# Performance work log

Measured on AMD Instinct MI355X. Metric: run time of the kernel, lower is better.

Reference implementation:

```python
import jax, jax.numpy as jnp
import numpy as np

EPS_NORM = 1e-12
RMS_EPS = 1e-5


def _rmsnorm(x, w):
    var = jnp.mean(jnp.square(x), axis=-1, keepdims=True)
    return x * jax.lax.rsqrt(var + RMS_EPS) * w


def setup_inputs() -> dict:
    key = jax.random.key(0)
    B, T, D, H, R, K = 2, 512, 1024, 16, 32, 3
    d = D // H
    ks = jax.random.split(key, 11)
    s = 0.02
    return dict(
        x=jax.random.normal(ks[0], (B, T, D), jnp.float32),
        Wq=jax.random.normal(ks[1], (D, D), jnp.float32) * s,
        Wk=jax.random.normal(ks[2], (D, D), jnp.float32) * s,
        Wv=jax.random.normal(ks[3], (D, D), jnp.float32) * s,
        Wo=jax.random.normal(ks[4], (D, D), jnp.float32) * s,
        wA=jax.random.normal(ks[5], (D, R), jnp.float32) * s,
        wB=jax.random.normal(ks[6], (R, D), jnp.float32) * s,
        conv_w=jax.random.normal(ks[7], (D, K), jnp.float32) * 0.5,
        beta_w=jax.random.normal(ks[8], (D, H), jnp.float32) * s,
        g_w=jax.random.normal(ks[9], (D, H), jnp.float32) * s,
        g_b=jnp.zeros((H,), jnp.float32),
        qnorm_w=jnp.ones((d,), jnp.float32),
        knorm_w=jnp.ones((d,), jnp.float32),
    )


def _path_attention(x, Wq, Wk, Wv, Wo, wA, wB, conv_w, beta_w, g_w, g_b, qnorm_w, knorm_w):
    # PaTH attention: s_ij = q_i^T (H_i ... H_{j+1}) k_j / sqrt(d) + (G_i - G_j),
    # H_t = I - beta_t w_t w_t^T (unit w_t), G = cumsum(logsigmoid(forget gate)).
    B, T, D = x.shape
    d = qnorm_w.shape[0]
    H = D // d
    scale = d ** -0.5

    q = (x @ Wq).reshape(B, T, H, d)
    k = (x @ Wk).reshape(B, T, H, d)
    v = (x @ Wv).reshape(B, T, H, d)

    # low-rank W projection + causal depthwise short conv (size 3) + silu
    w = (x @ wA) @ wB                                      # [B,T,D]
    wp = jnp.pad(w, ((0, 0), (2, 0), (0, 0)))
    w = wp[:, 0:T] * conv_w[:, 0] + wp[:, 1:T + 1] * conv_w[:, 1] + wp[:, 2:T + 2] * conv_w[:, 2]
    w = jax.nn.silu(w).reshape(B, T, H, d)
    # unit Householder directions
    w = w * jax.lax.rsqrt(jnp.sum(jnp.square(w), -1, keepdims=True) + EPS_NORM)

    beta = 2.0 * jax.nn.sigmoid(x @ beta_w)                # [B,T,H], in (0,2)
    g = jax.nn.log_sigmoid(x @ g_w + g_b)                  # [B,T,H] forget gate, log-space

    q = _rmsnorm(q, qnorm_w)
    k = _rmsnorm(k, knorm_w)

    # -> [B,H,T,(d)]
    q, k, v, w = (t.transpose(0, 2, 1, 3) for t in (q, k, v, w))
    beta = beta.transpose(0, 2, 1)
    g = g.transpose(0, 2, 1)

    # UT/WY form: A_{t,j} = w_t . (H_{t-1}...H_{j+1} k_j), t > j, via unit-lower tri solve:
    #   A_{t,j} + sum_{s<t} beta_s (w_t.w_s) A_{s,j} = (w_t.k_j) [t>j]
    tri_s = jnp.tril(jnp.ones((T, T), bool), -1)
    C = jnp.einsum('bhtd,bhsd->bhts', w, w) * beta[:, :, None, :]
    L = jnp.where(tri_s, C, 0.0) + jnp.eye(T, dtype=x.dtype)
    Rhs = jnp.where(tri_s, jnp.einsum('bhtd,bhjd->bhtj', w, k), 0.0)
    A = jax.scipy.linalg.solve_triangular(L, Rhs, lower=True, unit_diagonal=True)

    # s_ij = q_i.k_j - sum_{j<t<=i} (q_i.w_t) beta_t A_{t,j}
    tri = jnp.tril(jnp.ones((T, T), bool))
    qw = jnp.where(tri, jnp.einsum('bhid,bhtd->bhit', q, w), 0.0)
    S = jnp.einsum('bhid,bhjd->bhij', q, k) - jnp.einsum('bhit,bhtj->bhij', qw, beta[..., None] * A)

    G = jnp.cumsum(g, axis=-1)                             # [B,H,T]
    logits = S * scale + (G[..., :, None] - G[..., None, :])
    logits = jnp.where(tri, logits, -1e30)
    P = jax.nn.softmax(logits, axis=-1)
    o = jnp.einsum('bhij,bhjd->bhid', P, v)
    return o.transpose(0, 2, 1, 3).reshape(B, T, D) @ Wo


def reference(x, Wq, Wk, Wv, Wo, wA, wB, conv_w, beta_w, g_w, g_b, qnorm_w, knorm_w):
    return _path_attention(x, Wq, Wk, Wv, Wo, wA, wB, conv_w, beta_w, g_w, g_b, qnorm_w, knorm_w)
```

## Files before the change

### kernel.cpp

```cpp
#include <hip/hip_runtime.h>
#include <hip/hip_bf16.h>
#include <math.h>

#define B_ 2
#define T_ 512
#define D_ 1024
#define H_ 16
#define R_ 32
#define DH 64
#define BT_ (B_*T_)
#define BH_ (B_*H_)

typedef __attribute__((ext_vector_type(8))) short bf16x8;
typedef __attribute__((ext_vector_type(4))) short s16x4;
typedef __attribute__((ext_vector_type(4))) float f32x4;

#define MFMA_BF16(a, b, c) __builtin_amdgcn_mfma_f32_16x16x32_bf16(a, b, c, 0, 0, 0)

static __device__ __forceinline__ short bf16s(float v) {
  __hip_bfloat16 b = __float2bfloat16(v);
  return *reinterpret_cast<short*>(&b);
}
static __device__ __forceinline__ float b2f(__hip_bfloat16 h) { return __bfloat162float(h); }

__device__ __forceinline__ bf16x8 ldfrag(const __hip_bfloat16 s[][72], int b16, int kb, int fr, int kq) {
  return *(const bf16x8*)&s[b16 * 16 + fr][kb * 32 + kq * 8];
}
__device__ __forceinline__ void stage64(const __hip_bfloat16* __restrict__ g, int ldg,
                                        __hip_bfloat16 s[][72], int tid) {
#pragma unroll
  for (int l = 0; l < 2; ++l) {
    int f = tid + l * 256;
    int r = f >> 3, c = (f & 7) << 3;
    *(int4*)&s[r][c] = *(const int4*)&g[(size_t)r * ldg + c];
  }
}

typedef const __attribute__((address_space(1))) void* as1cv;
typedef __attribute__((address_space(3))) void* as3v;
__device__ __forceinline__ void gl16(const __hip_bfloat16* g, __hip_bfloat16* l) {
  __builtin_amdgcn_global_load_lds((as1cv)g, (as3v)l, 16, 0, 0);
}
__device__ __forceinline__ void stage64s(const __hip_bfloat16* __restrict__ g, int ldg,
                                         __hip_bfloat16* s, int tid) {
#pragma unroll
  for (int i = 0; i < 2; ++i) {
    int chunk = tid + i * 256;
    int r = chunk >> 3, c8 = (chunk & 7) ^ (r & 7);
    gl16(g + (size_t)r * ldg + c8 * 8, s + chunk * 8);
  }
}
__device__ __forceinline__ bf16x8 ldfragS(const __hip_bfloat16* s, int b16, int half, int fr, int kq) {
  int r = b16 * 16 + fr;
  int col8 = ((kq + half * 4) ^ (r & 7)) * 8;
  return *(const bf16x8*)&s[r * 64 + col8];
}

__global__ __launch_bounds__(256) void prep_k(const float* __restrict__ x,
                                              const float* __restrict__ Wq,
                                              const float* __restrict__ Wk,
                                              const float* __restrict__ Wv,
                                              const float* __restrict__ Wo,
                                              const float* __restrict__ wA,
                                              const float* __restrict__ bw,
                                              const float* __restrict__ gw,
                                              __hip_bfloat16* __restrict__ xhi,
                                              __hip_bfloat16* __restrict__ xlo,
                                              __hip_bfloat16* __restrict__ wqkvT,
                                              __hip_bfloat16* __restrict__ woT,
                                              __hip_bfloat16* __restrict__ wcThi,
                                              __hip_bfloat16* __restrict__ wcTlo) {
  __shared__ float tile[64][65];
  const int bid = blockIdx.x, tid = threadIdx.x;
  if (bid < 512) {
    int i8 = bid * 256 + tid;
    float4 v0 = ((const float4*)x)[i8 * 2];
    float4 v1 = ((const float4*)x)[i8 * 2 + 1];
    float c[8] = {v0.x, v0.y, v0.z, v0.w, v1.x, v1.y, v1.z, v1.w};
    bf16x8 ph, pl;
#pragma unroll
    for (int u = 0; u < 8; ++u) {
      __hip_bfloat16 h = __float2bfloat16(c[u]);
      ph[u] = *reinterpret_cast<short*>(&h);
      pl[u] = bf16s(c[u] - __bfloat162float(h));
    }
    *(bf16x8*)&xhi[(size_t)i8 * 8] = ph;
    *(bf16x8*)&xlo[(size_t)i8 * 8] = pl;
  } else if (bid < 1536) {
    const int zz = (bid - 512) >> 8, idx = (bid - 512) & 255;
    const float* Wm = (zz == 0) ? Wq : (zz == 1) ? Wk : (zz == 2) ? Wv : Wo;
    __hip_bfloat16* thi = (zz < 3) ? (wqkvT + (size_t)zz * 1024 * D_) : woT;
    const int bn = (idx & 15) * 64, bk = (idx >> 4) * 64;
#pragma unroll
    for (int l = 0; l < 4; ++l) {
      int f = tid + l * 256; int r = f >> 4, c = (f & 15) << 2;
      *(float4*)&tile[r][c] = *(const float4*)&Wm[(size_t)(bk + r) * D_ + bn + c];
    }
    __syncthreads();
#pragma unroll
    for (int l = 0; l < 4; ++l) {
      int f = tid + l * 256; int n = f >> 4, k0 = (f & 15) << 2;
      s16x4 ph;
#pragma unroll
      for (int u = 0; u < 4; ++u) ph[u] = bf16s(tile[k0 + u][n]);
      *(s16x4*)&thi[(size_t)(bn + n) * D_ + bk + k0] = ph;
    }
  } else {
    int n = bid - 1536;
    for (int k = tid; k < D_; k += 256) {
      float v;
      if (n < 32) v = wA[(size_t)k * R_ + n];
      else if (n < 48) v = bw[(size_t)k * H_ + (n - 32)];
      else v = gw[(size_t)k * H_ + (n - 48)];
      __hip_bfloat16 h = __float2bfloat16(v);
      wcThi[(size_t)n * D_ + k] = h;
      wcTlo[(size_t)n * D_ + k] = __float2bfloat16(v - __bfloat162float(h));
    }
  }
}

__global__ __launch_bounds__(256) void gemm_qkv(const __hip_bfloat16* __restrict__ ah,
                                                const __hip_bfloat16* __restrict__ bT,
                                                __hip_bfloat16* __restrict__ qb,
                                                __hip_bfloat16* __restrict__ kb,
                                                __hip_bfloat16* __restrict__ vhi,
                                                const float* __restrict__ qnw,
                                                const float* __restrict__ knw) {
  __shared__ __hip_bfloat16 As[2][64][64];
  __shared__ __hip_bfloat16 Bs[2][64][64];
  __shared__ __hip_bfloat16 Lt[64][72];
  const int bm = blockIdx.y * 64, bn = blockIdx.x * 64;
  const int tid = threadIdx.x, w = tid >> 6, lane = tid & 63;
  const int fr = lane & 15, kq = lane >> 4;
  const f32x4 zf = {0.f, 0.f, 0.f, 0.f};
  f32x4 acc[4] = {zf, zf, zf, zf};
  const __hip_bfloat16* ap = ah + (size_t)bm * D_;
  const __hip_bfloat16* bp = bT + (size_t)bn * D_;
  stage64s(ap, D_, &As[0][0][0], tid);
  stage64s(bp, D_, &Bs[0][0][0], tid);
  __syncthreads();
  for (int t = 0; t < 16; ++t) {
    const int cur = t & 1;
    if (t < 15) {
      stage64s(ap + (t + 1) * 64, D_, &As[cur ^ 1][0][0], tid);
      stage64s(bp + (t + 1) * 64, D_, &Bs[cur ^ 1][0][0], tid);
    }
    bf16x8 a0 = ldfragS(&As[cur][0][0], w, 0, fr, kq);
    bf16x8 a1 = ldfragS(&As[cur][0][0], w, 1, fr, kq);
#pragma unroll
    for (int n = 0; n < 4; ++n) {
      acc[n] = MFMA_BF16(a0, ldfragS(&Bs[cur][0][0], n, 0, fr, kq), acc[n]);
      acc[n] = MFMA_BF16(a1, ldfragS(&Bs[cur][0][0], n, 1, fr, kq), acc[n]);
    }
    __syncthreads();
  }

  if (bn < 2048) {
    float rs[4];
#pragma unroll
    for (int reg = 0; reg < 4; ++reg) {
      float s = 0.f;
#pragma unroll
      for (int n = 0; n < 4; ++n) s += acc[n][reg] * acc[n][reg];
#pragma unroll
      for (int mm = 1; mm <= 8; mm <<= 1) s += __shfl_xor(s, mm);
      rs[reg] = rsqrtf(s * (1.f / DH) + 1e-5f);
    }
    const bool isq = (bn < 1024);
    __hip_bfloat16* outp = isq ? qb : kb;
#pragma unroll
    for (int n = 0; n < 4; ++n) {
      int gn = bn + n * 16 + fr;
      int dd = gn & 63, h = (gn & 1023) >> 6;
      float nw = (isq ? qnw : knw)[dd];
#pragma unroll
      for (int reg = 0; reg < 4; ++reg) {
        int gm = bm + w * 16 + kq * 4 + reg;
        int bb = gm >> 9, tt = gm & 511;
        outp[(((size_t)(bb * H_ + h)) * T_ + tt) * DH + dd] =
            __float2bfloat16(acc[n][reg] * rs[reg] * nw);
      }
    }
  } else {
    const int row0 = w * 16 + kq * 4;
#pragma unroll
    for (int n = 0; n < 4; ++n) {
      int dd = n * 16 + fr;
#pragma unroll
      for (int reg = 0; reg < 4; ++reg) Lt[dd][row0 + reg] = __float2bfloat16(acc[n][reg]);
    }
    __syncthreads();
    const int b = bm >> 9, t0 = bm & 511, h = (bn - 2048) >> 6;
    const size_t base = ((size_t)(b * H_ + h)) * DH * T_;
#pragma unroll
    for (int l = 0; l < 2; ++l) {
      int f = tid + l * 256;
      int dd = f >> 3, tq = (f & 7) * 8;
      *(bf16x8*)&vhi[base + (size_t)dd * T_ + t0 + tq] = *(const bf16x8*)&Lt[dd][tq];
    }
  }
}

__global__ __launch_bounds__(256) void gemm_o(const __hip_bfloat16* __restrict__ ah,
                                              const __hip_bfloat16* __restrict__ bT,
                                              float* __restrict__ C) {
  __shared__ __hip_bfloat16 As[2][64][64];
  __shared__ __hip_bfloat16 Bs[2][64][64];
  const int bm = blockIdx.y * 64, bn = blockIdx.x * 64;
  const int tid = threadIdx.x, w = tid >> 6, lane = tid & 63;
  const int fr = lane & 15, kq = lane >> 4;
  const f32x4 zf = {0.f, 0.f, 0.f, 0.f};
  f32x4 acc[4] = {zf, zf, zf, zf};
  const __hip_bfloat16* ap = ah + (size_t)bm * D_;
  const __hip_bfloat16* bp = bT + (size_t)bn * D_;
  stage64s(ap, D_, &As[0][0][0], tid);
  stage64s(bp, D_, &Bs[0][0][0], tid);
  __syncthreads();
  for (int t = 0; t < 16; ++t) {
    const int cur = t & 1;
    if (t < 15) {
      stage64s(ap + (t + 1) * 64, D_, &As[cur ^ 1][0][0], tid);
      stage64s(bp + (t + 1) * 64, D_, &Bs[cur ^ 1][0][0], tid);
    }
    bf16x8 a0 = ldfragS(&As[cur][0][0], w, 0, fr, kq);
    bf16x8 a1 = ldfragS(&As[cur][0][0], w, 1, fr, kq);
#pragma unroll
    for (int n = 0; n < 4; ++n) {
      acc[n] = MFMA_BF16(a0, ldfragS(&Bs[cur][0][0], n, 0, fr, kq), acc[n]);
      acc[n] = MFMA_BF16(a1, ldfragS(&Bs[cur][0][0], n, 1, fr, kq), acc[n]);
    }
    __syncthreads();
  }
#pragma unroll
  for (int n = 0; n < 4; ++n) {
    int gn = bn + n * 16 + fr;
#pragma unroll
    for (int reg = 0; reg < 4; ++reg) {
      int gm = bm + w * 16 + kq * 4 + reg;
      C[(size_t)gm * D_ + gn] = acc[n][reg];
    }
  }
}

__global__ __launch_bounds__(256) void gemm_ycat(const __hip_bfloat16* __restrict__ ah,
                                                 const __hip_bfloat16* __restrict__ al,
                                                 const __hip_bfloat16* __restrict__ bh,
                                                 const __hip_bfloat16* __restrict__ bl,
                                                 float* __restrict__ ypart) {
  __shared__ __hip_bfloat16 Ah[64][72], Al[64][72], Bh[64][72], Bl[64][72];
  const int z = blockIdx.x, bm = blockIdx.y * 64;
  const int tid = threadIdx.x, w = tid >> 6, lane = tid & 63;
  const int fr = lane & 15, kq = lane >> 4;
  const f32x4 zf = {0.f, 0.f, 0.f, 0.f};
  f32x4 acc[4] = {zf, zf, zf, zf};
  float* C = ypart + (size_t)z * (BT_ * 64);
  for (int k0 = z * 256; k0 < z * 256 + 256; k0 += 64) {
    __syncthreads();
    stage64(ah + (size_t)bm * D_ + k0, D_, Ah, tid);
    stage64(al + (size_t)bm * D_ + k0, D_, Al, tid);
    stage64(bh + k0, D_, Bh, tid);
    stage64(bl + k0, D_, Bl, tid);
    __syncthreads();
    bf16x8 ah0 = ldfrag(Ah, w, 0, fr, kq), ah1 = ldfrag(Ah, w, 1, fr, kq);
    bf16x8 al0 = ldfrag(Al, w, 0, fr, kq), al1 = ldfrag(Al, w, 1, fr, kq);
#pragma unroll
    for (int nb = 0; nb < 4; ++nb) {
      bf16x8 b0 = ldfrag(Bh, nb, 0, fr, kq), b1 = ldfrag(Bh, nb, 1, fr, kq);
      bf16x8 c0 = ldfrag(Bl, nb, 0, fr, kq), c1 = ldfrag(Bl, nb, 1, fr, kq);
      acc[nb] = MFMA_BF16(ah0, b0, acc[nb]); acc[nb] = MFMA_BF16(ah1, b1, acc[nb]);
      acc[nb] = MFMA_BF16(ah0, c0, acc[nb]); acc[nb] = MFMA_BF16(ah1, c1, acc[nb]);
      acc[nb] = MFMA_BF16(al0, b0, acc[nb]); acc[nb] = MFMA_BF16(al1, b1, acc[nb]);
    }
  }
#pragma unroll
  for (int nb = 0; nb < 4; ++nb) {
    int n = nb * 16 + fr;
#pragma unroll
    for (int reg = 0; reg < 4; ++reg) {
      int m = bm + w * 16 + kq * 4 + reg;
      C[(size_t)m * 64 + n] = acc[nb][reg];
    }
  }
}

__global__ __launch_bounds__(512) void gate_wdir(const float* __restrict__ ypart,
                                                 const float* __restrict__ gb,
                                                 const float* __restrict__ wB,
                                                 const float* __restrict__ convw,
                                                 float* __restrict__ beta,
                                                 float* __restrict__ G,
                                                 float* __restrict__ wT,
                                                 __hip_bfloat16* __restrict__ wb16) {
  __shared__ float shm[T_];
  const int bid = blockIdx.x, tid = threadIdx.x;
  if (bid < BT_) {
    int bt = bid, b = bt / T_, t = bt - b * T_;
    float* wl = shm;
    if (tid < 3 * R_) {
      int row = tid / R_, r = tid - row * R_;
      int ts = t - row;
      float a = 0.f;
      if (ts >= 0) {
#pragma unroll
        for (int z = 0; z < 4; ++z)
          a += ypart[(size_t)z * (BT_ * 64) + (size_t)(b * T_ + ts) * 64 + r];
      }
      wl[row * R_ + r] = a;
    }
    __syncthreads();
#pragma unroll
    for (int half = 0; half < 2; ++half) {
      int col = tid + half * 512;
      float f0 = 0.f, f1 = 0.f, f2 = 0.f;
      for (int r = 0; r < R_; ++r) {
        float wb = wB[(size_t)r * D_ + col];
        f0 += wl[0 * R_ + r] * wb; f1 += wl[1 * R_ + r] * wb; f2 += wl[2 * R_ + r] * wb;
      }
      float y = f2 * convw[col * 3 + 0] + f1 * convw[col * 3 + 1] + f0 * convw[col * 3 + 2];
      float s = y / (1.f + expf(-y));
      float ss = s * s;
#pragma unroll
      for (int m = 32; m >= 1; m >>= 1) ss += __shfl_xor(ss, m);
      float outv = s * rsqrtf(ss + 1e-12f);
      int h = col >> 6, dd = col & 63;
      size_t o = (((size_t)(b * H_ + h)) * T_ + t) * DH + dd;
      wT[o] = outv;
      wb16[o] = __float2bfloat16(outv);
    }
  } else {
    int bh = bid - BT_, b = bh >> 4, h = bh & 15, t = tid;
    int bt = b * T_ + t;
    float by = 0.f, gy = gb[h];
#pragma unroll
    for (int z = 0; z < 4; ++z) {
      const float* yp = ypart + (size_t)z * (BT_ * 64) + (size_t)bt * 64;
      by += yp[32 + h];
      gy += yp[48 + h];
    }
    beta[(size_t)bh * T_ + t] = 2.f / (1.f + expf(-by));
    shm[t] = fminf(gy, 0.f) - log1pf(expf(-fabsf(gy)));
    __syncthreads();
    for (int off = 1; off < T_; off <<= 1) {
      float v = (t >= off) ? shm[t - off] : 0.f;
      __syncthreads();
      shm[t] += v;
      __syncthreads();
    }
    G[(size_t)bh * T_ + t] = shm[t];
  }
}

__global__ __launch_bounds__(256) void linv_k(const float* __restrict__ wT,
                                              const float* __restrict__ beta,
                                              __hip_bfloat16* __restrict__ linv) {
  __shared__ float Wsh[64][68];
  __shared__ float Csh[64][65];
  __shared__ float Li[64][68];
  __shared__ float bI[64];
  const int I = blockIdx.x, bhx = blockIdx.y;
  const int tid = threadIdx.x;
#pragma unroll
  for (int l = 0; l < 4; ++l) {
    int f = tid + l * 256; int r = f >> 4, c = (f & 15) << 2;
    *(float4*)&Wsh[r][c] = *(const float4*)&wT[((size_t)bhx * T_ + I * 64 + r) * DH + c];
  }
  if (tid < 64) bI[tid] = beta[(size_t)bhx * T_ + I * 64 + tid];
#pragma unroll
  for (int l = 0; l < 16; ++l) {
    int e = tid + l * 256; int r = e >> 6, c = e & 63;
    Li[r][c] = (r == c) ? 1.f : 0.f;
  }
  __syncthreads();
  const int tm = (tid >> 4) << 2, tn = (tid & 15) << 2;
  float cc[4][4] = {};
  for (int dd = 0; dd < 64; ++dd) {
    float a0 = Wsh[tm + 0][dd], a1 = Wsh[tm + 1][dd], a2 = Wsh[tm + 2][dd], a3 = Wsh[tm + 3][dd];
    float b0 = Wsh[tn + 0][dd], b1 = Wsh[tn + 1][dd], b2 = Wsh[tn + 2][dd], b3 = Wsh[tn + 3][dd];
    cc[0][0] += a0 * b0; cc[0][1] += a0 * b1; cc[0][2] += a0 * b2; cc[0][3] += a0 * b3;
    cc[1][0] += a1 * b0; cc[1][1] += a1 * b1; cc[1][2] += a1 * b2; cc[1][3] += a1 * b3;
    cc[2][0] += a2 * b0; cc[2][1] += a2 * b1; cc[2][2] += a2 * b2; cc[2][3] += a2 * b3;
    cc[3][0] += a3 * b0; cc[3][1] += a3 * b1; cc[3][2] += a3 * b2; cc[3][3] += a3 * b3;
  }
#pragma unroll
  for (int ii = 0; ii < 4; ++ii)
#pragma unroll
    for (int jj = 0; jj < 4; ++jj)
      Csh[tm + ii][tn + jj] = (tm + ii > tn + jj) ? cc[ii][jj] * bI[tn + jj] : 0.f;
  __syncthreads();
  const int sL = tid & 63, g = tid >> 6;
  for (int r0 = 0; r0 < 64; r0 += 8) {
    float a[8];
#pragma unroll
    for (int u = 0; u < 8; ++u) a[u] = Li[r0 + u][sL];
    __syncthreads();
#pragma unroll
    for (int u = 1; u < 8; ++u)
#pragma unroll
      for (int s = 0; s < u; ++s) a[u] -= Csh[r0 + u][r0 + s] * a[s];
    if (g == 0) {
#pragma unroll
      for (int u = 1; u < 8; ++u) Li[r0 + u][sL] = a[u];
    }
    for (int r2 = r0 + 8 + g; r2 < 64; r2 += 4) {
      float acc = Li[r2][sL];
#pragma unroll
      for (int u = 0; u < 8; ++u) acc -= Csh[r2][r0 + u] * a[u];
      Li[r2][sL] = acc;
    }
    __syncthreads();
  }
#pragma unroll
  for (int l = 0; l < 4; ++l) {
    int f = tid + l * 256; int r = f >> 4, c0 = (f & 15) << 2;
    s16x4 p;
    p.x = bf16s(Li[r][c0 + 0]); p.y = bf16s(Li[r][c0 + 1]);
    p.z = bf16s(Li[r][c0 + 2]); p.w = bf16s(Li[r][c0 + 3]);
    *(s16x4*)&linv[((size_t)(bhx * 8 + I)) * 4096 + r * 64 + c0] = p;
  }
}

__global__ __launch_bounds__(256) void chain_k(const __hip_bfloat16* __restrict__ kb,
                                               const __hip_bfloat16* __restrict__ wb,
                                               const __hip_bfloat16* __restrict__ linv,
                                               const float* __restrict__ beta,
                                               __hip_bfloat16* __restrict__ abT,
                                               __hip_bfloat16* __restrict__ khat) {
  __shared__ __hip_bfloat16 Kb[64][72];
  __shared__ __hip_bfloat16 Ws[64][72];
  __shared__ __hip_bfloat16 WsT[64][72];
  __shared__ __hip_bfloat16 Ls[64][72];
  __shared__ __hip_bfloat16 Kh[64][72];
  __shared__ __hip_bfloat16 Ps[64][72];
  __shared__ __hip_bfloat16 Xs[64][72];
  __shared__ float bI[64];
  const int ch = blockIdx.x, bhx = blockIdx.y;
  const int tid = threadIdx.x, w = tid >> 6, lane = tid & 63;
  const int fr = lane & 15, kq = lane >> 4;
  const int jr = w * 16 + kq * 4;
  const size_t hb = (size_t)bhx * T_;
  const f32x4 zf = {0.f, 0.f, 0.f, 0.f};

  stage64(kb + (hb + ch * 64) * DH, DH, Kb, tid);
  f32x4 macc[4] = {zf, zf, zf, zf};

  for (int I = ch; I < 8; ++I) {
    __syncthreads();
    stage64(wb + (hb + I * 64) * DH, DH, Ws, tid);
    stage64(linv + ((size_t)(bhx * 8 + I)) * 4096, 64, Ls, tid);
    if (tid < 64) bI[tid] = beta[hb + I * 64 + tid];
#pragma unroll
    for (int nb = 0; nb < 4; ++nb) {
      int d = nb * 16 + fr;
#pragma unroll
      for (int reg = 0; reg < 4; ++reg)
        Kh[jr + reg][d] = __float2bfloat16(b2f(Kb[jr + reg][d]) - macc[nb][reg]);
    }
    __syncthreads();
#pragma unroll
    for (int l = 0; l < 2; ++l) {
      int f = tid + l * 256;
      int r = f >> 3, c = (f & 7) << 3;
      *(int4*)&khat[(((size_t)(bhx * 8 + I)) * T_ + ch * 64 + r) * DH + c] = *(const int4*)&Kh[r][c];
    }
#pragma unroll
    for (int l = 0; l < 16; ++l) {
      int e = tid + l * 256;
      int t = e >> 6, d = e & 63;
      WsT[d][t] = Ws[t][d];
    }
    bf16x8 kh0 = ldfrag(Kh, w, 0, fr, kq), kh1 = ldfrag(Kh, w, 1, fr, kq);
    f32x4 pt[4];
#pragma unroll
    for (int nb = 0; nb < 4; ++nb) {
      pt[nb] = MFMA_BF16(kh0, ldfrag(Ws, nb, 0, fr, kq), zf);
      pt[nb] = MFMA_BF16(kh1, ldfrag(Ws, nb, 1, fr, kq), pt[nb]);
    }
#pragma unroll
    for (int nb = 0; nb < 4; ++nb) {
      int t = nb * 16 + fr;
#pragma unroll
      for (int reg = 0; reg < 4; ++reg) {
        float v = pt[nb][reg];
        if (I == ch && t <= jr + reg) v = 0.f;
        Ps[jr + reg][t] = __float2bfloat16(v);
      }
    }
    __syncthreads();
    bf16x8 la0 = ldfrag(Ls, w, 0, fr, kq), la1 = ldfrag(Ls, w, 1, fr, kq);
    f32x4 av[4];
#pragma unroll
    for (int nb = 0; nb < 4; ++nb) {
      av[nb] = MFMA_BF16(la0, ldfrag(Ps, nb, 0, fr, kq), zf);
      av[nb] = MFMA_BF16(la1, ldfrag(Ps, nb, 1, fr, kq), av[nb]);
    }
#pragma unroll
    for (int nb = 0; nb < 4; ++nb) {
      s16x4 p;
      p.x = bf16s(bI[jr + 0] * av[nb][0]);
      p.y = bf16s(bI[jr + 1] * av[nb][1]);
      p.z = bf16s(bI[jr + 2] * av[nb][2]);
      p.w = bf16s(bI[jr + 3] * av[nb][3]);
      *(s16x4*)&Xs[nb * 16 + fr][jr] = p;
    }
    __syncthreads();
#pragma unroll
    for (int l = 0; l < 2; ++l) {
      int f = tid + l * 256;
      int r = f >> 3, c = (f & 7) << 3;
      *(int4*)&abT[(hb + ch * 64 + r) * T_ + I * 64 + c] = *(const int4*)&Xs[r][c];
    }
    bf16x8 xa0 = ldfrag(Xs, w, 0, fr, kq), xa1 = ldfrag(Xs, w, 1, fr, kq);
#pragma unroll
    for (int nb = 0; nb < 4; ++nb) {
      macc[nb] = MFMA_BF16(xa0, ldfrag(WsT, nb, 0, fr, kq), macc[nb]);
      macc[nb] = MFMA_BF16(xa1, ldfrag(WsT, nb, 1, fr, kq), macc[nb]);
    }
  }
}

__global__ __launch_bounds__(256) void attn_fused(const __hip_bfloat16* __restrict__ qb,
                                                  const __hip_bfloat16* __restrict__ wb,
                                                  const __hip_bfloat16* __restrict__ khat,
                                                  const __hip_bfloat16* __restrict__ abT,
                                                  const __hip_bfloat16* __restrict__ vhi,
                                                  const float* __restrict__ G,
                                                  __hip_bfloat16* __restrict__ ohi) {
  __shared__ __hip_bfloat16 Ms[64][72];
  __shared__ __hip_bfloat16 Ks[64][72];
  __shared__ __hip_bfloat16 Cs[64][72];
  __shared__ __hip_bfloat16 Vh[64][72];
  __shared__ __hip_bfloat16 Ps[64][72];
  const int it = blockIdx.x, bh = blockIdx.y;
  const int b = bh >> 4, h = bh & 15;
  const int tid = threadIdx.x, w = tid >> 6, lane = tid & 63;
  const int fr = lane & 15, kq = lane >> 4;
  const int row0 = w * 16 + kq * 4;
  const size_t hb = (size_t)bh * T_;
  const f32x4 zero = {0.f, 0.f, 0.f, 0.f};

  stage64(qb + (hb + it * 64) * DH, DH, Ks, tid);
  stage64(wb + (hb + it * 64) * DH, DH, Cs, tid);
  __syncthreads();
  const bf16x8 a0 = ldfrag(Ks, w, 0, fr, kq);
  const bf16x8 a1 = ldfrag(Ks, w, 1, fr, kq);
  f32x4 qw[4];
#pragma unroll
  for (int nb = 0; nb < 4; ++nb) {
    qw[nb] = MFMA_BF16(a0, ldfrag(Cs, nb, 0, fr, kq), zero);
    qw[nb] = MFMA_BF16(a1, ldfrag(Cs, nb, 1, fr, kq), qw[nb]);
  }
#pragma unroll
  for (int nb = 0; nb < 4; ++nb) {
    int col = nb * 16 + fr;
#pragma unroll
    for (int reg = 0; reg < 4; ++reg) {
      float v = -qw[nb][reg];
      if (col > row0 + reg) v = 0.f;
      Ms[row0 + reg][col] = __float2bfloat16(v);
    }
  }
  __syncthreads();
  const bf16x8 m0 = ldfrag(Ms, w, 0, fr, kq);
  const bf16x8 m1 = ldfrag(Ms, w, 1, fr, kq);

  float Gi[4];
#pragma unroll
  for (int reg = 0; reg < 4; ++reg) Gi[reg] = G[hb + it * 64 + row0 + reg];
  float mrow[4] = {-3e38f, -3e38f, -3e38f, -3e38f};
  float lrow[4] = {0.f, 0.f, 0.f, 0.f};
  f32x4 acc_o[4] = {zero, zero, zero, zero};
  const __hip_bfloat16* kh = khat + ((size_t)(bh * 8 + it)) * T_ * DH;

  for (int jt = 0; jt <= it; ++jt) {
    __syncthreads();
    stage64(kh + (size_t)(jt * 64) * DH, DH, Ks, tid);
    stage64(abT + (hb + jt * 64) * T_ + it * 64, T_, Cs, tid);
    stage64(vhi + (size_t)bh * DH * T_ + jt * 64, T_, Vh, tid);
    __syncthreads();
    f32x4 acc[4];
#pragma unroll
    for (int nb = 0; nb < 4; ++nb) {
      acc[nb] = MFMA_BF16(a0, ldfrag(Ks, nb, 0, fr, kq), zero);
      acc[nb] = MFMA_BF16(a1, ldfrag(Ks, nb, 1, fr, kq), acc[nb]);
      acc[nb] = MFMA_BF16(m0, ldfrag(Cs, nb, 0, fr, kq), acc[nb]);
      acc[nb] = MFMA_BF16(m1, ldfrag(Cs, nb, 1, fr, kq), acc[nb]);
    }
    float gj[4];
#pragma unroll
    for (int nb = 0; nb < 4; ++nb) gj[nb] = G[hb + jt * 64 + nb * 16 + fr];
    const bool diag = (jt == it);
    float vv[4][4];
#pragma unroll
    for (int reg = 0; reg < 4; ++reg) {
      float tm = -3e38f;
#pragma unroll
      for (int nb = 0; nb < 4; ++nb) {
        float vx = acc[nb][reg] * 0.125f + Gi[reg] - gj[nb];
        if (diag && (nb * 16 + fr) > row0 + reg) vx = -3e38f;
        vv[nb][reg] = vx;
        tm = fmaxf(tm, vx);
      }
#pragma unroll
      for (int mm = 1; mm <= 8; mm <<= 1) tm = fmaxf(tm, __shfl_xor(tm, mm));
      float mnew = fmaxf(mrow[reg], tm);
      float sc = __expf(mrow[reg] - mnew);
      mrow[reg] = mnew;
      float tsum = 0.f;
#pragma unroll
      for (int nb = 0; nb < 4; ++nb) {
        float p = __expf(vv[nb][reg] - mnew);
        Ps[row0 + reg][nb * 16 + fr] = __float2bfloat16(p);
        tsum += p;
      }
#pragma unroll
      for (int mm = 1; mm <= 8; mm <<= 1) tsum += __shfl_xor(tsum, mm);
      lrow[reg] = lrow[reg] * sc + tsum;
#pragma unroll
      for (int nb = 0; nb < 4; ++nb) acc_o[nb][reg] *= sc;
    }
    __syncthreads();
    const bf16x8 p0 = ldfrag(Ps, w, 0, fr, kq);
    const bf16x8 p1 = ldfrag(Ps, w, 1, fr, kq);
#pragma unroll
    for (int nb = 0; nb < 4; ++nb) {
      acc_o[nb] = MFMA_BF16(p0, ldfrag(Vh, nb, 0, fr, kq), acc_o[nb]);
      acc_o[nb] = MFMA_BF16(p1, ldfrag(Vh, nb, 1, fr, kq), acc_o[nb]);
    }
  }
#pragma unroll
  for (int reg = 0; reg < 4; ++reg) {
    float inv = 1.f / lrow[reg];
    int i = it * 64 + row0 + reg;
#pragma unroll
    for (int nb = 0; nb < 4; ++nb) {
      int dd = nb * 16 + fr;
      size_t oi = ((size_t)(b * T_ + i)) * D_ + h * 64 + dd;
      ohi[oi] = __float2bfloat16(acc_o[nb][reg] * inv);
    }
  }
}

extern "C" void kernel_launch(void* const* d_in, const int* in_sizes, int n_in,
                              void* d_out, int out_size, void* d_ws, size_t ws_size,
                              hipStream_t stream) {
  (void)in_sizes; (void)n_in; (void)out_size; (void)ws_size;
  const float* x     = (const float*)d_in[0];
  const float* Wq    = (const float*)d_in[1];
  const float* Wk    = (const float*)d_in[2];
  const float* Wv    = (const float*)d_in[3];
  const float* Wo    = (const float*)d_in[4];
  const float* wA    = (const float*)d_in[5];
  const float* wB    = (const float*)d_in[6];
  const float* convw = (const float*)d_in[7];
  const float* bw    = (const float*)d_in[8];
  const float* gw    = (const float*)d_in[9];
  const float* gb    = (const float*)d_in[10];
  const float* qnw   = (const float*)d_in[11];
  const float* knw   = (const float*)d_in[12];

  const size_t N1 = (size_t)BT_ * D_;
  const size_t NTT = (size_t)BH_ * T_ * T_;
  float* ws = (float*)d_ws;
  float* wTb   = ws;
  float* ypart = wTb + N1;
  float* beta  = ypart + (size_t)4 * BT_ * 64;
  float* G     = beta + (size_t)BH_ * T_;
  __hip_bfloat16* qb16  = (__hip_bfloat16*)(G + (size_t)BH_ * T_);
  __hip_bfloat16* kb16  = qb16 + N1;
  __hip_bfloat16* wb16  = kb16 + N1;
  __hip_bfloat16* abT   = wb16 + N1;
  __hip_bfloat16* linvb = abT + NTT;
  __hip_bfloat16* xhi   = linvb + (size_t)BH_ * 8 * 4096;
  __hip_bfloat16* xlo   = xhi + N1;
  __hip_bfloat16* obhi  = xlo + N1;
  __hip_bfloat16* woThi = obhi + N1;
  __hip_bfloat16* vhi   = woThi + N1;
  __hip_bfloat16* wcThi = vhi + N1;
  __hip_bfloat16* wcTlo = wcThi + (size_t)64 * D_;
  __hip_bfloat16* khat  = wcTlo + (size_t)64 * D_;
  __hip_bfloat16* wqkvT = khat + (size_t)BH_ * 8 * T_ * DH;

  prep_k<<<1600, 256, 0, stream>>>(x, Wq, Wk, Wv, Wo, wA, bw, gw,
                                   xhi, xlo, wqkvT, woThi, wcThi, wcTlo);
  gemm_ycat<<<dim3(4, 16), 256, 0, stream>>>(xhi, xlo, wcThi, wcTlo, ypart);
  gemm_qkv<<<dim3(48, 16), 256, 0, stream>>>(xhi, wqkvT, qb16, kb16, vhi, qnw, knw);
  gate_wdir<<<BT_ + BH_, 512, 0, stream>>>(ypart, gb, wB, convw, beta, G, wTb, wb16);
  linv_k<<<dim3(8, BH_), 256, 0, stream>>>(wTb, beta, linvb);
  chain_k<<<dim3(8, BH_), 256, 0, stream>>>(kb16, wb16, linvb, beta, abT, khat);
  attn_fused<<<dim3(8, BH_), 256, 0, stream>>>(qb16, wb16, khat, abT, vhi, G, obhi);
  gemm_o<<<dim3(16, 16), 256, 0, stream>>>(obhi, woThi, (float*)d_out);
}
```

Before: 120.1 us.

## Merge ycat into qkv GEMM launch and split long causal attention rows

The separate low-rank ycat GEMM is folded into the QKV GEMM grid as four extra column blocks, which removes one kernel launch and lets both run concurrently. The attention kernel now uses a task table so the four longest query tiles (it 4..7) are each split into two KV ranges, giving more balanced work per block. Partial outputs and their max/sum statistics go to workspace and are combined by a new attn_merge kernel. This adds an extra launch plus fp32 partial-output traffic in exchange for better load balance across the causal triangle.

Measured after the change: 111.5 us. 1.08x faster.

```diff
diff --git a/kernel.cpp b/kernel.cpp
--- a/kernel.cpp
+++ b/kernel.cpp
@@ -22,6 +22,11 @@
   return *reinterpret_cast<short*>(&b);
 }
 static __device__ __forceinline__ float b2f(__hip_bfloat16 h) { return __bfloat162float(h); }
+
+__constant__ int ATT_IT[12]   = {0,1,2,3,4,4,5,5,6,6,7,7};
+__constant__ int ATT_J0[12]   = {0,0,0,0,0,3,0,3,0,4,0,4};
+__constant__ int ATT_J1[12]   = {0,1,2,3,2,4,2,5,3,6,3,7};
+__constant__ int ATT_PART[12] = {-1,-1,-1,-1,0,1,0,1,0,1,0,1};
 
 __device__ __forceinline__ bf16x8 ldfrag(const __hip_bfloat16 s[][72], int b16, int kb, int fr, int kq) {
   return *(const bf16x8*)&s[b16 * 16 + fr][kb * 32 + kq * 8];
@@ -119,84 +124,126 @@
   }
 }
 
-__global__ __launch_bounds__(256) void gemm_qkv(const __hip_bfloat16* __restrict__ ah,
-                                                const __hip_bfloat16* __restrict__ bT,
-                                                __hip_bfloat16* __restrict__ qb,
-                                                __hip_bfloat16* __restrict__ kb,
-                                                __hip_bfloat16* __restrict__ vhi,
-                                                const float* __restrict__ qnw,
-                                                const float* __restrict__ knw) {
-  __shared__ __hip_bfloat16 As[2][64][64];
-  __shared__ __hip_bfloat16 Bs[2][64][64];
-  __shared__ __hip_bfloat16 Lt[64][72];
-  const int bm = blockIdx.y * 64, bn = blockIdx.x * 64;
+__global__ __launch_bounds__(256) void gemm_qkv_ycat(const __hip_bfloat16* __restrict__ ah,
+                                                     const __hip_bfloat16* __restrict__ al,
+                                                     const __hip_bfloat16* __restrict__ bT,
+                                                     const __hip_bfloat16* __restrict__ wch,
+                                                     const __hip_bfloat16* __restrict__ wcl,
+                                                     __hip_bfloat16* __restrict__ qb,
+                                                     __hip_bfloat16* __restrict__ kb,
+                                                     __hip_bfloat16* __restrict__ vhi,
+                                                     float* __restrict__ ypart,
+                                                     const float* __restrict__ qnw,
+                                                     const float* __restrict__ knw) {
+  __shared__ __align__(16) char smem[43008];
+  const int bx = blockIdx.x, bm = blockIdx.y * 64;
   const int tid = threadIdx.x, w = tid >> 6, lane = tid & 63;
   const int fr = lane & 15, kq = lane >> 4;
   const f32x4 zf = {0.f, 0.f, 0.f, 0.f};
   f32x4 acc[4] = {zf, zf, zf, zf};
-  const __hip_bfloat16* ap = ah + (size_t)bm * D_;
-  const __hip_bfloat16* bp = bT + (size_t)bn * D_;
-  stage64s(ap, D_, &As[0][0][0], tid);
-  stage64s(bp, D_, &Bs[0][0][0], tid);
-  __syncthreads();
-  for (int t = 0; t < 16; ++t) {
-    const int cur = t & 1;
-    if (t < 15) {
-      stage64s(ap + (t + 1) * 64, D_, &As[cur ^ 1][0][0], tid);
-      stage64s(bp + (t + 1) * 64, D_, &Bs[cur ^ 1][0][0], tid);
-    }
-    bf16x8 a0 = ldfragS(&As[cur][0][0], w, 0, fr, kq);
-    bf16x8 a1 = ldfragS(&As[cur][0][0], w, 1, fr, kq);
-#pragma unroll
-    for (int n = 0; n < 4; ++n) {
-      acc[n] = MFMA_BF16(a0, ldfragS(&Bs[cur][0][0], n, 0, fr, kq), acc[n]);
-      acc[n] = MFMA_BF16(a1, ldfragS(&Bs[cur][0][0], n, 1, fr, kq), acc[n]);
-    }
-    __syncthreads();
-  }
-
-  if (bn < 2048) {
-    float rs[4];
-#pragma unroll
-    for (int reg = 0; reg < 4; ++reg) {
-      float s = 0.f;
-#pragma unroll
-      for (int n = 0; n < 4; ++n) s += acc[n][reg] * acc[n][reg];
-#pragma unroll
-      for (int mm = 1; mm <= 8; mm <<= 1) s += __shfl_xor(s, mm);
-      rs[reg] = rsqrtf(s * (1.f / DH) + 1e-5f);
-    }
-    const bool isq = (bn < 1024);
-    __hip_bfloat16* outp = isq ? qb : kb;
-#pragma unroll
-    for (int n = 0; n < 4; ++n) {
-      int gn = bn + n * 16 + fr;
-      int dd = gn & 63, h = (gn & 1023) >> 6;
-      float nw = (isq ? qnw : knw)[dd];
+
+  if (bx < 48) {
+    __hip_bfloat16* As = (__hip_bfloat16*)smem;
+    __hip_bfloat16* Bs = As + 2 * 4096;
+    __hip_bfloat16 (*Lt)[72] = (__hip_bfloat16(*)[72])(Bs + 2 * 4096);
+    const int bn = bx * 64;
+    const __hip_bfloat16* ap = ah + (size_t)bm * D_;
+    const __hip_bfloat16* bp = bT + (size_t)bn * D_;
+    stage64s(ap, D_, As, tid);
+    stage64s(bp, D_, Bs, tid);
+    __syncthreads();
+    for (int t = 0; t < 16; ++t) {
+      const int cur = t & 1;
+      if (t < 15) {
+        stage64s(ap + (t + 1) * 64, D_, As + (cur ^ 1) * 4096, tid);
+        stage64s(bp + (t + 1) * 64, D_, Bs + (cur ^ 1) * 4096, tid);
+      }
+      bf16x8 a0 = ldfragS(As + cur * 4096, w, 0, fr, kq);
+      bf16x8 a1 = ldfragS(As + cur * 4096, w, 1, fr, kq);
+#pragma unroll
+      for (int n = 0; n < 4; ++n) {
+        acc[n] = MFMA_BF16(a0, ldfragS(Bs + cur * 4096, n, 0, fr, kq), acc[n]);
+        acc[n] = MFMA_BF16(a1, ldfragS(Bs + cur * 4096, n, 1, fr, kq), acc[n]);
+      }
+      __syncthreads();
+    }
+    if (bn < 2048) {
+      float rs[4];
 #pragma unroll
       for (int reg = 0; reg < 4; ++reg) {
-        int gm = bm + w * 16 + kq * 4 + reg;
-        int bb = gm >> 9, tt = gm & 511;
-        outp[(((size_t)(bb * H_ + h)) * T_ + tt) * DH + dd] =
-            __float2bfloat16(acc[n][reg] * rs[reg] * nw);
+        float s = 0.f;
+#pragma unroll
+        for (int n = 0; n < 4; ++n) s += acc[n][reg] * acc[n][reg];
+#pragma unroll
+        for (int mm = 1; mm <= 8; mm <<= 1) s += __shfl_xor(s, mm);
+        rs[reg] = rsqrtf(s * (1.f / DH) + 1e-5f);
+      }
+      const bool isq = (bn < 1024);
+      __hip_bfloat16* outp = isq ? qb : kb;
+#pragma unroll
+      for (int n = 0; n < 4; ++n) {
+        int gn = bn + n * 16 + fr;
+        int dd = gn & 63, h = (gn & 1023) >> 6;
+        float nw = (isq ? qnw : knw)[dd];
+#pragma unroll
+        for (int reg = 0; reg < 4; ++reg) {
+          int gm = bm + w * 16 + kq * 4 + reg;
+          int bb = gm >> 9, tt = gm & 511;
+          outp[(((size_t)(bb * H_ + h)) * T_ + tt) * DH + dd] =
+              __float2bfloat16(acc[n][reg] * rs[reg] * nw);
+        }
+      }
+    } else {
+      const int row0 = w * 16 + kq * 4;
+#pragma unroll
+      for (int n = 0; n < 4; ++n) {
+        int dd = n * 16 + fr;
+#pragma unroll
+        for (int reg = 0; reg < 4; ++reg) Lt[dd][row0 + reg] = __float2bfloat16(acc[n][reg]);
+      }
+      __syncthreads();
+      const int b = bm >> 9, t0 = bm & 511, h = (bn - 2048) >> 6;
+      const size_t base = ((size_t)(b * H_ + h)) * DH * T_;
+#pragma unroll
+      for (int l = 0; l < 2; ++l) {
+        int f = tid + l * 256;
+        int dd = f >> 3, tq = (f & 7) * 8;
+        *(bf16x8*)&vhi[base + (size_t)dd * T_ + t0 + tq] = *(const bf16x8*)&Lt[dd][tq];
       }
     }
   } else {
-    const int row0 = w * 16 + kq * 4;
-#pragma unroll
-    for (int n = 0; n < 4; ++n) {
-      int dd = n * 16 + fr;
-#pragma unroll
-      for (int reg = 0; reg < 4; ++reg) Lt[dd][row0 + reg] = __float2bfloat16(acc[n][reg]);
-    }
-    __syncthreads();
-    const int b = bm >> 9, t0 = bm & 511, h = (bn - 2048) >> 6;
-    const size_t base = ((size_t)(b * H_ + h)) * DH * T_;
-#pragma unroll
-    for (int l = 0; l < 2; ++l) {
-      int f = tid + l * 256;
-      int dd = f >> 3, tq = (f & 7) * 8;
-      *(bf16x8*)&vhi[base + (size_t)dd * T_ + t0 + tq] = *(const bf16x8*)&Lt[dd][tq];
+    __hip_bfloat16 (*Ah)[72] = (__hip_bfloat16(*)[72])smem;
+    __hip_bfloat16 (*Al)[72] = (__hip_bfloat16(*)[72])(smem + 9216);
+    __hip_bfloat16 (*Bh)[72] = (__hip_bfloat16(*)[72])(smem + 18432);
+    __hip_bfloat16 (*Bl)[72] = (__hip_bfloat16(*)[72])(smem + 27648);
+    const int z = bx - 48;
+    float* C = ypart + (size_t)z * (BT_ * 64);
+    for (int k0 = z * 256; k0 < z * 256 + 256; k0 += 64) {
+      __syncthreads();
+      stage64(ah + (size_t)bm * D_ + k0, D_, Ah, tid);
+      stage64(al + (size_t)bm * D_ + k0, D_, Al, tid);
+      stage64(wch + k0, D_, Bh, tid);
+      stage64(wcl + k0, D_, Bl, tid);
+      __syncthreads();
+      bf16x8 ah0 = ldfrag(Ah, w, 0, fr, kq), ah1 = ldfrag(Ah, w, 1, fr, kq);
+      bf16x8 al0 = ldfrag(Al, w, 0, fr, kq), al1 = ldfrag(Al, w, 1, fr, kq);
+#pragma unroll
+      for (int nb = 0; nb < 4; ++nb) {
+        bf16x8 b0 = ldfrag(Bh, nb, 0, fr, kq), b1 = ldfrag(Bh, nb, 1, fr, kq);
+        bf16x8 c0 = ldfrag(Bl, nb, 0, fr, kq), c1 = ldfrag(Bl, nb, 1, fr, kq);
+        acc[nb] = MFMA_BF16(ah0, b0, acc[nb]); acc[nb] = MFMA_BF16(ah1, b1, acc[nb]);
+        acc[nb] = MFMA_BF16(ah0, c0, acc[nb]); acc[nb] = MFMA_BF16(ah1, c1, acc[nb]);
+        acc[nb] = MFMA_BF16(al0, b0, acc[nb]); acc[nb] = MFMA_BF16(al1, b1, acc[nb]);
+      }
+    }
+#pragma unroll
+    for (int nb = 0; nb < 4; ++nb) {
+      int n = nb * 16 + fr;
+#pragma unroll
+      for (int reg = 0; reg < 4; ++reg) {
+        int m = bm + w * 16 + kq * 4 + reg;
+        C[(size_t)m * 64 + n] = acc[nb][reg];
+      }
     }
   }
 }
@@ -242,47 +289,6 @@
   }
 }
 
-__global__ __launch_bounds__(256) void gemm_ycat(const __hip_bfloat16* __restrict__ ah,
-                                                 const __hip_bfloat16* __restrict__ al,
-                                                 const __hip_bfloat16* __restrict__ bh,
-                                                 const __hip_bfloat16* __restrict__ bl,
-                                                 float* __restrict__ ypart) {
-  __shared__ __hip_bfloat16 Ah[64][72], Al[64][72], Bh[64][72], Bl[64][72];
-  const int z = blockIdx.x, bm = blockIdx.y * 64;
-  const int tid = threadIdx.x, w = tid >> 6, lane = tid & 63;
-  const int fr = lane & 15, kq = lane >> 4;
-  const f32x4 zf = {0.f, 0.f, 0.f, 0.f};
-  f32x4 acc[4] = {zf, zf, zf, zf};
-  float* C = ypart + (size_t)z * (BT_ * 64);
-  for (int k0 = z * 256; k0 < z * 256 + 256; k0 += 64) {
-    __syncthreads();
-    stage64(ah + (size_t)bm * D_ + k0, D_, Ah, tid);
-    stage64(al + (size_t)bm * D_ + k0, D_, Al, tid);
-    stage64(bh + k0, D_, Bh, tid);
-    stage64(bl + k0, D_, Bl, tid);
-    __syncthreads();
-    bf16x8 ah0 = ldfrag(Ah, w, 0, fr, kq), ah1 = ldfrag(Ah, w, 1, fr, kq);
-    bf16x8 al0 = ldfrag(Al, w, 0, fr, kq), al1 = ldfrag(Al, w, 1, fr, kq);
-#pragma unroll
-    for (int nb = 0; nb < 4; ++nb) {
-      bf16x8 b0 = ldfrag(Bh, nb, 0, fr, kq), b1 = ldfrag(Bh, nb, 1, fr, kq);
-      bf16x8 c0 = ldfrag(Bl, nb, 0, fr, kq), c1 = ldfrag(Bl, nb, 1, fr, kq);
-      acc[nb] = MFMA_BF16(ah0, b0, acc[nb]); acc[nb] = MFMA_BF16(ah1, b1, acc[nb]);
-      acc[nb] = MFMA_BF16(ah0, c0, acc[nb]); acc[nb] = MFMA_BF16(ah1, c1, acc[nb]);
-      acc[nb] = MFMA_BF16(al0, b0, acc[nb]); acc[nb] = MFMA_BF16(al1, b1, acc[nb]);
-    }
-  }
-#pragma unroll
-  for (int nb = 0; nb < 4; ++nb) {
-    int n = nb * 16 + fr;
-#pragma unroll
-    for (int reg = 0; reg < 4; ++reg) {
-      int m = bm + w * 16 + kq * 4 + reg;
-      C[(size_t)m * 64 + n] = acc[nb][reg];
-    }
-  }
-}
-
 __global__ __launch_bounds__(512) void gate_wdir(const float* __restrict__ ypart,
                                                  const float* __restrict__ gb,
                                                  const float* __restrict__ wB,
@@ -524,13 +530,16 @@
                                                   const __hip_bfloat16* __restrict__ abT,
                                                   const __hip_bfloat16* __restrict__ vhi,
                                                   const float* __restrict__ G,
-                                                  __hip_bfloat16* __restrict__ ohi) {
+                                                  __hip_bfloat16* __restrict__ ohi,
+                                                  float* __restrict__ opart,
+                                                  float* __restrict__ mlbuf) {
   __shared__ __hip_bfloat16 Ms[64][72];
   __shared__ __hip_bfloat16 Ks[64][72];
   __shared__ __hip_bfloat16 Cs[64][72];
   __shared__ __hip_bfloat16 Vh[64][72];
   __shared__ __hip_bfloat16 Ps[64][72];
-  const int it = blockIdx.x, bh = blockIdx.y;
+  const int task = blockIdx.x, bh = blockIdx.y;
+  const int it = ATT_IT[task], j0 = ATT_J0[task], j1 = ATT_J1[task], part = ATT_PART[task];
   const int b = bh >> 4, h = bh & 15;
   const int tid = threadIdx.x, w = tid >> 6, lane = tid & 63;
   const int fr = lane & 15, kq = lane >> 4;
@@ -571,7 +580,7 @@
   f32x4 acc_o[4] = {zero, zero, zero, zero};
   const __hip_bfloat16* kh = khat + ((size_t)(bh * 8 + it)) * T_ * DH;
 
-  for (int jt = 0; jt <= it; ++jt) {
+  for (int jt = j0; jt <= j1; ++jt) {
     __syncthreads();
     stage64(kh + (size_t)(jt * 64) * DH, DH, Ks, tid);
     stage64(abT + (hb + jt * 64) * T_ + it * 64, T_, Cs, tid);
@@ -627,16 +636,61 @@
       acc_o[nb] = MFMA_BF16(p1, ldfrag(Vh, nb, 1, fr, kq), acc_o[nb]);
     }
   }
-#pragma unroll
-  for (int reg = 0; reg < 4; ++reg) {
-    float inv = 1.f / lrow[reg];
-    int i = it * 64 + row0 + reg;
-#pragma unroll
-    for (int nb = 0; nb < 4; ++nb) {
-      int dd = nb * 16 + fr;
-      size_t oi = ((size_t)(b * T_ + i)) * D_ + h * 64 + dd;
-      ohi[oi] = __float2bfloat16(acc_o[nb][reg] * inv);
-    }
+  if (part < 0) {
+#pragma unroll
+    for (int reg = 0; reg < 4; ++reg) {
+      float inv = 1.f / lrow[reg];
+      int i = it * 64 + row0 + reg;
+#pragma unroll
+      for (int nb = 0; nb < 4; ++nb) {
+        int dd = nb * 16 + fr;
+        size_t oi = ((size_t)(b * T_ + i)) * D_ + h * 64 + dd;
+        ohi[oi] = __float2bfloat16(acc_o[nb][reg] * inv);
+      }
+    }
+  } else {
+    const size_t pb = ((size_t)(bh * 4 + (it - 4)) * 2 + part);
+    float* Op = opart + pb * 4096;
+    float* mlp = mlbuf + pb * 128;
+#pragma unroll
+    for (int reg = 0; reg < 4; ++reg) {
+      int row = row0 + reg;
+#pragma unroll
+      for (int nb = 0; nb < 4; ++nb) {
+        Op[row * 64 + nb * 16 + fr] = acc_o[nb][reg];
+      }
+      if (fr == 0) {
+        mlp[row] = mrow[reg];
+        mlp[64 + row] = lrow[reg];
+      }
+    }
+  }
+}
+
+__global__ __launch_bounds__(256) void attn_merge(const float* __restrict__ opart,
+                                                  const float* __restrict__ mlbuf,
+                                                  __hip_bfloat16* __restrict__ ohi) {
+  const int idx = blockIdx.x;
+  const int bh = idx >> 2, it = (idx & 3) + 4;
+  const int b = bh >> 4, h = bh & 15;
+  const int tid = threadIdx.x;
+  const float* O0 = opart + ((size_t)idx * 2 + 0) * 4096;
+  const float* O1 = opart + ((size_t)idx * 2 + 1) * 4096;
+  const float* ml0 = mlbuf + ((size_t)idx * 2 + 0) * 128;
+  const float* ml1 = mlbuf + ((size_t)idx * 2 + 1) * 128;
+  const int row = tid >> 2, dd0 = (tid & 3) * 16;
+  const float m0 = ml0[row], l0 = ml0[64 + row];
+  const float m1 = ml1[row], l1 = ml1[64 + row];
+  const float m = fmaxf(m0, m1);
+  const float e0 = __expf(m0 - m), e1 = __expf(m1 - m);
+  const float inv = 1.f / (l0 * e0 + l1 * e1);
+  const int i = it * 64 + row;
+  const size_t ob = ((size_t)(b * T_ + i)) * D_ + h * 64;
+#pragma unroll
+  for (int u = 0; u < 16; ++u) {
+    int dd = dd0 + u;
+    float v = (O0[row * 64 + dd] * e0 + O1[row * 64 + dd] * e1) * inv;
+    ohi[ob + dd] = __float2bfloat16(v);
   }
 }
 
@@ -665,7 +719,9 @@
   float* ypart = wTb + N1;
   float* beta  = ypart + (size_t)4 * BT_ * 64;
   float* G     = beta + (size_t)BH_ * T_;
-  __hip_bfloat16* qb16  = (__hip_bfloat16*)(G + (size_t)BH_ * T_);
+  float* opart = G + (size_t)BH_ * T_;
+  float* mlbuf = opart + (size_t)BH_ * 4 * 2 * 4096;
+  __hip_bfloat16* qb16  = (__hip_bfloat16*)(mlbuf + (size_t)BH_ * 4 * 2 * 128);
   __hip_bfloat16* kb16  = qb16 + N1;
   __hip_bfloat16* wb16  = kb16 + N1;
   __hip_bfloat16* abT   = wb16 + N1;
@@ -682,11 +738,13 @@
 
   prep_k<<<1600, 256, 0, stream>>>(x, Wq, Wk, Wv, Wo, wA, bw, gw,
                                    xhi, xlo, wqkvT, woThi, wcThi, wcTlo);
-  gemm_ycat<<<dim3(4, 16), 256, 0, stream>>>(xhi, xlo, wcThi, wcTlo, ypart);
-  gemm_qkv<<<dim3(48, 16), 256, 0, stream>>>(xhi, wqkvT, qb16, kb16, vhi, qnw, knw);
+  gemm_qkv_ycat<<<dim3(52, 16), 256, 0, stream>>>(xhi, xlo, wqkvT, wcThi, wcTlo,
+                                                  qb16, kb16, vhi, ypart, qnw, knw);
   gate_wdir<<<BT_ + BH_, 512, 0, stream>>>(ypart, gb, wB, convw, beta, G, wTb, wb16);
   linv_k<<<dim3(8, BH_), 256, 0, stream>>>(wTb, beta, linvb);
   chain_k<<<dim3(8, BH_), 256, 0, stream>>>(kb16, wb16, linvb, beta, abT, khat);
-  attn_fused<<<dim3(8, BH_), 256, 0, stream>>>(qb16, wb16, khat, abT, vhi, G, obhi);
+  attn_fused<<<dim3(12, BH_), 256, 0, stream>>>(qb16, wb16, khat, abT, vhi, G,
+                                                obhi, opart, mlbuf);
+  attn_merge<<<128, 256, 0, stream>>>(opart, mlbuf, obhi);
   gemm_o<<<dim3(16, 16), 256, 0, stream>>>(obhi, woThi, (float*)d_out);
 }
```
